# Optimization experiments

Measured on AMD Instinct MI355X. Metric: run time of the kernel, lower is better.

## Reference

```python
import jax, jax.numpy as jnp
import numpy as np

EMBED_DIM = 1024
NUM_HEADS = 16
HEAD_DIM = EMBED_DIM // NUM_HEADS
L, B, S = 2048, 2, 2048


def setup_inputs() -> dict:
    key = jax.random.key(0)
    k1, k2, k3, k4, k5, k6, k7 = jax.random.split(key, 7)
    query = jax.random.normal(k1, (L, B, EMBED_DIM), dtype=jnp.float32)
    kk = jax.random.normal(k2, (S, B, EMBED_DIM), dtype=jnp.float32)
    vv = jax.random.normal(k3, (S, B, EMBED_DIM), dtype=jnp.float32)
    # in_proj: Linear(E, 3E) -> weight (3E, E), bias (3E,)
    w_in = jax.random.normal(k4, (3 * EMBED_DIM, EMBED_DIM), dtype=jnp.float32) * (1.0 / np.sqrt(EMBED_DIM))
    b_in = jax.random.normal(k5, (3 * EMBED_DIM,), dtype=jnp.float32) * 0.02
    w_out = jax.random.normal(k6, (EMBED_DIM, EMBED_DIM), dtype=jnp.float32) * (1.0 / np.sqrt(EMBED_DIM))
    b_out = jax.random.normal(k7, (EMBED_DIM,), dtype=jnp.float32) * 0.02
    return {"query": query, "key": kk, "value": vv,
            "w_in": w_in, "b_in": b_in, "w_out": w_out, "b_out": b_out}


def _split_heads(x, seq_len, batch):
    # (T, B, E) -> (B, H, T, d)
    return x.reshape(seq_len, batch, NUM_HEADS, HEAD_DIM).transpose(1, 2, 0, 3)


def reference(query, key, value, w_in, b_in, w_out, b_out):
    seq_q, batch, _ = query.shape
    seq_kv = key.shape[0]
    # split fused in_proj into q/k/v projections (chunk along output rows)
    wq, wk, wv = jnp.split(w_in, 3, axis=0)
    bq, bk, bv = jnp.split(b_in, 3, axis=0)
    q = query @ wq.T + bq            # (L, B, E)
    k = key @ wk.T + bk              # (S, B, E)
    v = value @ wv.T + bv            # (S, B, E)
    q = _split_heads(q, seq_q, batch)   # (B, H, L, d)
    k = _split_heads(k, seq_kv, batch)  # (B, H, S, d)
    v = _split_heads(v, seq_kv, batch)  # (B, H, S, d)
    scale = jnp.asarray(np.sqrt(HEAD_DIM), dtype=q.dtype)
    scores = jnp.einsum('bhld,bhsd->bhls', q, k) / scale  # (B, H, L, S)
    attn = jax.nn.softmax(scores, axis=-1)
    context = jnp.einsum('bhls,bhsd->bhld', attn, v)      # (B, H, L, d)
    # (B, H, L, d) -> (L, B, E)
    context = context.transpose(2, 0, 1, 3).reshape(seq_q, batch, EMBED_DIM)
    attn_output = context @ w_out.T + b_out
    return attn_output
```

## Files before the change

### kernel.cpp

```cpp
#include <hip/hip_runtime.h>
#include <hip/hip_bf16.h>
#include <stdint.h>

#define L_SEQ 2048
#define S_SEQ 2048
#define BATCH 2
#define EMB 1024
#define NH 16
#define HD 64
#define MROWS 4096

typedef __bf16 bf16x8 __attribute__((ext_vector_type(8)));
typedef float f32x4 __attribute__((ext_vector_type(4)));
typedef __hip_bfloat16 bf16;

__device__ __forceinline__ f32x4 mfma16(bf16x8 a, bf16x8 b, f32x4 c) {
    return __builtin_amdgcn_mfma_f32_16x16x32_bf16(a, b, c, 0, 0, 0);
}

__device__ __forceinline__ void gll16(const bf16* g, bf16* l) {
    __builtin_amdgcn_global_load_lds(
        (const __attribute__((address_space(1))) void*)g,
        (__attribute__((address_space(3))) void*)l, 16, 0, 0);
}

__device__ __forceinline__ bf16x8 ld8_cvt(const float* p) {
    const float4 a = *reinterpret_cast<const float4*>(p);
    const float4 b = *reinterpret_cast<const float4*>(p + 4);
    union { bf16x8 v; bf16 h[8]; } u;
    u.h[0] = __float2bfloat16(a.x); u.h[1] = __float2bfloat16(a.y);
    u.h[2] = __float2bfloat16(a.z); u.h[3] = __float2bfloat16(a.w);
    u.h[4] = __float2bfloat16(b.x); u.h[5] = __float2bfloat16(b.y);
    u.h[6] = __float2bfloat16(b.z); u.h[7] = __float2bfloat16(b.w);
    return u.v;
}

__device__ __forceinline__ uint32_t packbf2(float a, float b) {
    const uint32_t ra = __float_as_uint(a) + 0x8000u;
    const uint32_t rb = __float_as_uint(b) + 0x8000u;
    return __builtin_amdgcn_perm(rb, ra, 0x07060302u);
}

__global__ __launch_bounds__(256) void cvt_kernel(
    const float* __restrict__ w_in, const float* __restrict__ w_out,
    const float* __restrict__ q_in, const float* __restrict__ k_in,
    const float* __restrict__ v_in,
    bf16* __restrict__ wib, bf16* __restrict__ wob,
    bf16* __restrict__ Xq, bf16* __restrict__ Xk, bf16* __restrict__ Xv)
{
    const size_t i = ((size_t)blockIdx.x * 256 + threadIdx.x) * 8;
    const size_t o1 = (size_t)3 * EMB * EMB;
    const size_t o2 = o1 + (size_t)EMB * EMB;
    const size_t o3 = o2 + (size_t)MROWS * EMB;
    const size_t o4 = o3 + (size_t)MROWS * EMB;
    const float* src; bf16* dst; size_t j;
    if      (i < o1) { src = w_in;  dst = wib; j = i; }
    else if (i < o2) { src = w_out; dst = wob; j = i - o1; }
    else if (i < o3) { src = q_in;  dst = Xq;  j = i - o2; }
    else if (i < o4) { src = k_in;  dst = Xk;  j = i - o3; }
    else             { src = v_in;  dst = Xv;  j = i - o4; }
    *reinterpret_cast<bf16x8*>(dst + j) = ld8_cvt(src + j);
}

__global__ __launch_bounds__(256) void qkv_gemm(
    const bf16* __restrict__ Xq, const bf16* __restrict__ Xk,
    const bf16* __restrict__ Xv, const bf16* __restrict__ wib,
    const float* __restrict__ b_in,
    bf16* __restrict__ Qh, bf16* __restrict__ Kh, bf16* __restrict__ Vh)
{
    __shared__ alignas(16) bf16 lds_a[128 * 32];
    __shared__ alignas(16) bf16 lds_b[128 * 32];

    const int tid  = threadIdx.x;
    const int lane = tid & 63;
    const int wv   = tid >> 6;
    const int quad = lane >> 4;
    const int lx   = lane & 15;

    const int m0  = blockIdx.x * 128;
    const int n0g = blockIdx.y * 128;
    const int chunk = n0g >> 10;
    const bf16* Aop = (chunk == 0) ? Xq : (chunk == 1) ? Xk : Xv;

    const int wm = (wv >> 1) * 64;
    const int wn = (wv & 1) * 64;

    const int gr = 16 * wv + (lane >> 2);
    const int gc = (lane & 3) * 8;
    const bf16* gA = Aop + (size_t)(m0 + gr) * EMB + gc;
    const bf16* gB = wib + (size_t)(n0g + gr) * EMB + gc;
    bf16* lA = lds_a + wv * 512;
    bf16* lB = lds_b + wv * 512;

    f32x4 acc[4][4];
#pragma unroll
    for (int i = 0; i < 4; i++)
#pragma unroll
        for (int j = 0; j < 4; j++) acc[i][j] = (f32x4){0.f, 0.f, 0.f, 0.f};

    for (int kt = 0; kt < EMB; kt += 32) {
        __syncthreads();
        gll16(gA + kt, lA);
        gll16(gA + 64 * EMB + kt, lA + 2048);
        gll16(gB + kt, lB);
        gll16(gB + 64 * EMB + kt, lB + 2048);
        __syncthreads();

        bf16x8 af[4], bfv[4];
        const int ka = quad * 8;
#pragma unroll
        for (int sm = 0; sm < 4; sm++)
            af[sm] = *reinterpret_cast<const bf16x8*>(lds_a + (wm + sm * 16 + lx) * 32 + ka);
#pragma unroll
        for (int sn = 0; sn < 4; sn++)
            bfv[sn] = *reinterpret_cast<const bf16x8*>(lds_b + (wn + sn * 16 + lx) * 32 + ka);
#pragma unroll
        for (int sm = 0; sm < 4; sm++)
#pragma unroll
            for (int sn = 0; sn < 4; sn++)
                acc[sm][sn] = mfma16(af[sm], bfv[sn], acc[sm][sn]);
    }

    const float scale = (chunk == 0) ? 0.18033688011112042f : 1.0f;
    bf16* dst = (chunk == 0) ? Qh : (chunk == 1) ? Kh : Vh;
#pragma unroll
    for (int sn = 0; sn < 4; sn++) {
        const int n_g = n0g + wn + sn * 16 + lx;
        const float bias = b_in[n_g];
        const int nc = n_g & (EMB - 1);
        const int h  = nc >> 6;
        const int dd = nc & 63;
#pragma unroll
        for (int sm = 0; sm < 4; sm++) {
#pragma unroll
            for (int r = 0; r < 4; r++) {
                const int m_g = m0 + wm + sm * 16 + quad * 4 + r;
                const int t = m_g >> 1;
                const int b = m_g & 1;
                const int bhidx = b * NH + h;
                const float v = (acc[sm][sn][r] + bias) * scale;
                dst[((size_t)bhidx * S_SEQ + t) * HD + dd] = __float2bfloat16(v);
            }
        }
    }
}

#define TST 72
__global__ __launch_bounds__(256) void transpose_v(
    const bf16* __restrict__ Vh, bf16* __restrict__ Vt)
{
    __shared__ alignas(16) bf16 t[64 * TST];
    const int tid = threadIdx.x;
    const int bh  = blockIdx.y;
    const int s0  = blockIdx.x * 64;
    const int r0  = tid >> 3;
    const int c0  = (tid & 7) * 8;

    const bf16* src = Vh + (size_t)bh * S_SEQ * HD;
    uint4 a = *reinterpret_cast<const uint4*>(src + (size_t)(s0 + r0) * HD + c0);
    uint4 b = *reinterpret_cast<const uint4*>(src + (size_t)(s0 + r0 + 32) * HD + c0);
    *reinterpret_cast<uint4*>(t + r0 * TST + c0) = a;
    *reinterpret_cast<uint4*>(t + (r0 + 32) * TST + c0) = b;
    __syncthreads();

    const int sc = (tid & 7) * 8;
    bf16* dst = Vt + (size_t)bh * HD * S_SEQ;
#pragma unroll
    for (int half = 0; half < 2; half++) {
        const int d = (tid >> 3) + half * 32;
        union { bf16 h[8]; uint4 u; } o;
#pragma unroll
        for (int j = 0; j < 8; j++) o.h[j] = t[(sc + j) * TST + d];
        *reinterpret_cast<uint4*>(dst + (size_t)d * S_SEQ + s0 + sc) = o.u;
    }
}

__global__ __launch_bounds__(512, 4) void attn_kernel(
    const bf16* __restrict__ Qh, const bf16* __restrict__ Kh,
    const bf16* __restrict__ Vt, bf16* __restrict__ ctx)
{
    __shared__ alignas(16) bf16 k_lds[128 * 64];
    __shared__ alignas(16) bf16 v_lds[64 * 128];

    const int tid  = threadIdx.x;
    const int lane = tid & 63;
    const int wv   = tid >> 6;
    const int quad = lane >> 4;
    const int lx   = lane & 15;
    const int lx7  = lane & 7;

    const int bh = blockIdx.y;
    const int l0 = blockIdx.x * 128;
    const int q0 = wv * 16;

    const bf16* Kbase = Kh + (size_t)bh * S_SEQ * HD;
    const bf16* Vbase = Vt + (size_t)bh * HD * S_SEQ;

    const bf16* qrow = Qh + ((size_t)bh * L_SEQ + l0 + q0 + lx) * HD + quad * 8;
    const bf16x8 qf0 = *reinterpret_cast<const bf16x8*>(qrow);
    const bf16x8 qf1 = *reinterpret_cast<const bf16x8*>(qrow + 32);

    float m_run = -1e30f, l_run = 0.f;
    f32x4 accv[4];
#pragma unroll
    for (int sn = 0; sn < 4; sn++) accv[sn] = (f32x4){0.f, 0.f, 0.f, 0.f};

    const int kr0 = tid >> 3;
    const int kc  = (tid & 7) * 8;
    const int vd0 = tid >> 4;
    const int vs  = (tid & 15) * 8;
    const int ksw = (((kc >> 3) ^ (kr0 & 7)) << 3);
    const int vsw = (((vs >> 3) ^ (vd0 & 7)) << 3);

    uint4 ka = *reinterpret_cast<const uint4*>(Kbase + (size_t)kr0 * HD + kc);
    uint4 kb = *reinterpret_cast<const uint4*>(Kbase + (size_t)(kr0 + 64) * HD + kc);
    uint4 va = *reinterpret_cast<const uint4*>(Vbase + (size_t)vd0 * S_SEQ + vs);
    uint4 vb = *reinterpret_cast<const uint4*>(Vbase + (size_t)(vd0 + 32) * S_SEQ + vs);

    for (int s0 = 0; s0 < S_SEQ; s0 += 128) {
        __syncthreads();
        *reinterpret_cast<uint4*>(k_lds + kr0 * 64 + ksw) = ka;
        *reinterpret_cast<uint4*>(k_lds + (kr0 + 64) * 64 + ksw) = kb;
        *reinterpret_cast<uint4*>(v_lds + vd0 * 128 + vsw) = va;
        *reinterpret_cast<uint4*>(v_lds + (vd0 + 32) * 128 + vsw) = vb;
        __syncthreads();

        const int s1 = (s0 + 128) & (S_SEQ - 1);
        ka = *reinterpret_cast<const uint4*>(Kbase + (size_t)(s1 + kr0) * HD + kc);
        kb = *reinterpret_cast<const uint4*>(Kbase + (size_t)(s1 + kr0 + 64) * HD + kc);
        va = *reinterpret_cast<const uint4*>(Vbase + (size_t)vd0 * S_SEQ + s1 + vs);
        vb = *reinterpret_cast<const uint4*>(Vbase + (size_t)(vd0 + 32) * S_SEQ + s1 + vs);

        f32x4 sc[8];
#pragma unroll
        for (int c = 0; c < 8; c++) {
            const bf16* kr = k_lds + (c * 16 + lx) * 64;
            bf16x8 kf0 = *reinterpret_cast<const bf16x8*>(kr + ((quad ^ lx7) << 3));
            bf16x8 kf1 = *reinterpret_cast<const bf16x8*>(kr + (((quad + 4) ^ lx7) << 3));
            f32x4 tt = (f32x4){0.f, 0.f, 0.f, 0.f};
            tt = mfma16(kf0, qf0, tt);
            tt = mfma16(kf1, qf1, tt);
            sc[c] = tt;
        }

        f32x4 vm = sc[0];
#pragma unroll
        for (int c = 1; c < 8; c++)
#pragma unroll
            for (int r = 0; r < 4; r++) vm[r] = fmaxf(vm[r], sc[c][r]);
        float mloc = fmaxf(fmaxf(vm[0], vm[1]), fmaxf(vm[2], vm[3]));
        mloc = fmaxf(mloc, __shfl_xor(mloc, 16));
        mloc = fmaxf(mloc, __shfl_xor(mloc, 32));
        const float mnew = fmaxf(m_run, mloc);
        const float al = __builtin_amdgcn_exp2f(m_run - mnew);
        m_run = mnew;

        const f32x4 mnew4 = (f32x4){mnew, mnew, mnew, mnew};
        f32x4 rv = (f32x4){0.f, 0.f, 0.f, 0.f};
#pragma unroll
        for (int c = 0; c < 8; c++) {
            f32x4 d = sc[c] - mnew4;
#pragma unroll
            for (int r = 0; r < 4; r++) sc[c][r] = __builtin_amdgcn_exp2f(d[r]);
            rv += sc[c];
        }
        float rsum = (rv[0] + rv[1]) + (rv[2] + rv[3]);
        rsum += __shfl_xor(rsum, 16);
        rsum += __shfl_xor(rsum, 32);
        l_run = l_run * al + rsum;

#pragma unroll
        for (int r = 0; r < 4; r++) {
            const float ar = __shfl(al, quad * 20 + r);
#pragma unroll
            for (int sn = 0; sn < 4; sn++) accv[sn][r] *= ar;
        }

        uint32_t pk0[8], pk1[8];
#pragma unroll
        for (int c = 0; c < 8; c++) {
            pk0[c] = packbf2(sc[c][0], sc[c][1]);
            pk1[c] = packbf2(sc[c][2], sc[c][3]);
        }

#pragma unroll
        for (int sk = 0; sk < 4; sk++) {
            auto t0 = __builtin_amdgcn_permlane32_swap(pk0[2 * sk], pk0[2 * sk + 1], false, false);
            auto a02 = __builtin_amdgcn_permlane16_swap(t0[0], t0[1], false, false);
            auto t1 = __builtin_amdgcn_permlane32_swap(pk1[2 * sk], pk1[2 * sk + 1], false, false);
            auto a13 = __builtin_amdgcn_permlane16_swap(t1[0], t1[1], false, false);
            union { uint32_t u[4]; bf16x8 v; } pf;
            pf.u[0] = a02[0]; pf.u[1] = a13[0]; pf.u[2] = a02[1]; pf.u[3] = a13[1];
#pragma unroll
            for (int sn = 0; sn < 4; sn++) {
                const bf16* vr = v_lds + (sn * 16 + lx) * 128 + ((((sk * 4 + quad) ^ lx7)) << 3);
                accv[sn] = mfma16(pf.v, *reinterpret_cast<const bf16x8*>(vr), accv[sn]);
            }
        }
    }

    const int b = bh >> 4;
    const int h = bh & 15;
#pragma unroll
    for (int r = 0; r < 4; r++) {
        const float lr = __shfl(l_run, quad * 20 + r);
        const float inv = 1.f / lr;
        const int l = l0 + q0 + quad * 4 + r;
#pragma unroll
        for (int sn = 0; sn < 4; sn++) {
            const int dd = sn * 16 + lx;
            ctx[(size_t)(l * BATCH + b) * EMB + h * HD + dd] =
                __float2bfloat16(accv[sn][r] * inv);
        }
    }
}

__global__ __launch_bounds__(256) void out_gemm(
    const bf16* __restrict__ ctx, const bf16* __restrict__ wob,
    const float* __restrict__ b_out, float* __restrict__ out)
{
    __shared__ alignas(16) bf16 lds_a[64 * 32];
    __shared__ alignas(16) bf16 lds_b[128 * 32];

    const int tid  = threadIdx.x;
    const int lane = tid & 63;
    const int wv   = tid >> 6;
    const int quad = lane >> 4;
    const int lx   = lane & 15;

    const int m0 = blockIdx.x * 64;
    const int n0 = blockIdx.y * 128;

    const int wm = (wv >> 1) * 32;
    const int wn = (wv & 1) * 64;

    const int gr = 16 * wv + (lane >> 2);
    const int gc = (lane & 3) * 8;
    const bf16* gA = ctx + (size_t)(m0 + gr) * EMB + gc;
    const bf16* gB = wob + (size_t)(n0 + gr) * EMB + gc;
    bf16* lA = lds_a + wv * 512;
    bf16* lB = lds_b + wv * 512;

    f32x4 acc[2][4];
#pragma unroll
    for (int i = 0; i < 2; i++)
#pragma unroll
        for (int j = 0; j < 4; j++) acc[i][j] = (f32x4){0.f, 0.f, 0.f, 0.f};

    for (int kt = 0; kt < EMB; kt += 32) {
        __syncthreads();
        gll16(gA + kt, lA);
        gll16(gB + kt, lB);
        gll16(gB + 64 * EMB + kt, lB + 2048);
        __syncthreads();

        bf16x8 af[2], bfv[4];
        const int ka = quad * 8;
#pragma unroll
        for (int sm = 0; sm < 2; sm++)
            af[sm] = *reinterpret_cast<const bf16x8*>(lds_a + (wm + sm * 16 + lx) * 32 + ka);
#pragma unroll
        for (int sn = 0; sn < 4; sn++)
            bfv[sn] = *reinterpret_cast<const bf16x8*>(lds_b + (wn + sn * 16 + lx) * 32 + ka);
#pragma unroll
        for (int sm = 0; sm < 2; sm++)
#pragma unroll
            for (int sn = 0; sn < 4; sn++)
                acc[sm][sn] = mfma16(af[sm], bfv[sn], acc[sm][sn]);
    }

#pragma unroll
    for (int sn = 0; sn < 4; sn++) {
        const int n_g = n0 + wn + sn * 16 + lx;
        const float bias = b_out[n_g];
#pragma unroll
        for (int sm = 0; sm < 2; sm++) {
#pragma unroll
            for (int r = 0; r < 4; r++) {
                const int m_g = m0 + wm + sm * 16 + quad * 4 + r;
                out[(size_t)m_g * EMB + n_g] = acc[sm][sn][r] + bias;
            }
        }
    }
}

extern "C" void kernel_launch(void* const* d_in, const int* in_sizes, int n_in,
                              void* d_out, int out_size, void* d_ws, size_t ws_size,
                              hipStream_t stream)
{
    const float* query = (const float*)d_in[0];
    const float* key_  = (const float*)d_in[1];
    const float* value = (const float*)d_in[2];
    const float* w_in  = (const float*)d_in[3];
    const float* b_in  = (const float*)d_in[4];
    const float* w_out = (const float*)d_in[5];
    const float* b_out = (const float*)d_in[6];
    float* out = (float*)d_out;

    const size_t seg = (size_t)MROWS * EMB;
    bf16* wib = (bf16*)d_ws;
    bf16* wob = wib + (size_t)3 * EMB * EMB;
    bf16* Xq  = wob + (size_t)EMB * EMB;
    bf16* Xk  = Xq + seg;
    bf16* Xv  = Xk + seg;
    bf16* Qh  = Xv + seg;
    bf16* Kh  = Qh + seg;
    bf16* Vh  = Kh + seg;
    bf16* Vt  = Xq;
    bf16* ctx = Vh;

    cvt_kernel<<<8192, 256, 0, stream>>>(w_in, w_out, query, key_, value,
                                         wib, wob, Xq, Xk, Xv);
    qkv_gemm<<<dim3(32, 24), 256, 0, stream>>>(Xq, Xk, Xv, wib, b_in, Qh, Kh, Vh);
    transpose_v<<<dim3(32, 32), 256, 0, stream>>>(Vh, Vt);
    attn_kernel<<<dim3(16, 32), 512, 0, stream>>>(Qh, Kh, Vt, ctx);
    out_gemm<<<dim3(64, 8), 256, 0, stream>>>(ctx, wob, b_out, out);
}
```

Baseline: 235.4 us.

## Double-buffer K via async global-to-LDS loads and read V directly from global

```diff
diff --git a/kernel.cpp b/kernel.cpp
--- a/kernel.cpp
+++ b/kernel.cpp
@@ -179,8 +179,7 @@
     const bf16* __restrict__ Qh, const bf16* __restrict__ Kh,
     const bf16* __restrict__ Vt, bf16* __restrict__ ctx)
 {
-    __shared__ alignas(16) bf16 k_lds[128 * 64];
-    __shared__ alignas(16) bf16 v_lds[64 * 128];
+    __shared__ alignas(16) bf16 k_lds[2][128 * 64];
 
     const int tid  = threadIdx.x;
     const int lane = tid & 63;
@@ -205,42 +204,49 @@
 #pragma unroll
     for (int sn = 0; sn < 4; sn++) accv[sn] = (f32x4){0.f, 0.f, 0.f, 0.f};
 
-    const int kr0 = tid >> 3;
-    const int kc  = (tid & 7) * 8;
-    const int vd0 = tid >> 4;
-    const int vs  = (tid & 15) * 8;
-    const int ksw = (((kc >> 3) ^ (kr0 & 7)) << 3);
-    const int vsw = (((vs >> 3) ^ (vd0 & 7)) << 3);
-
-    uint4 ka = *reinterpret_cast<const uint4*>(Kbase + (size_t)kr0 * HD + kc);
-    uint4 kb = *reinterpret_cast<const uint4*>(Kbase + (size_t)(kr0 + 64) * HD + kc);
-    uint4 va = *reinterpret_cast<const uint4*>(Vbase + (size_t)vd0 * S_SEQ + vs);
-    uint4 vb = *reinterpret_cast<const uint4*>(Vbase + (size_t)(vd0 + 32) * S_SEQ + vs);
-
+    const int grow  = wv * 16 + (lane >> 3);
+    const int gcol8 = ((lane & 7) ^ (lane >> 3)) << 3;
+    const bf16* gK = Kbase + (size_t)grow * HD + gcol8;
+    bf16* lK0 = &k_lds[0][(wv * 16) * 64];
+    bf16* lK1 = &k_lds[1][(wv * 16) * 64];
+
+    const bf16* vBp[4];
+#pragma unroll
+    for (int sn = 0; sn < 4; sn++)
+        vBp[sn] = Vbase + (size_t)(sn * 16 + lx) * S_SEQ + quad * 8;
+
+    gll16(gK, lK0);
+    gll16(gK + (size_t)8 * HD, lK0 + 8 * 64);
+
+    int cur = 0;
     for (int s0 = 0; s0 < S_SEQ; s0 += 128) {
         __syncthreads();
-        *reinterpret_cast<uint4*>(k_lds + kr0 * 64 + ksw) = ka;
-        *reinterpret_cast<uint4*>(k_lds + (kr0 + 64) * 64 + ksw) = kb;
-        *reinterpret_cast<uint4*>(v_lds + vd0 * 128 + vsw) = va;
-        *reinterpret_cast<uint4*>(v_lds + (vd0 + 32) * 128 + vsw) = vb;
-        __syncthreads();
-
-        const int s1 = (s0 + 128) & (S_SEQ - 1);
-        ka = *reinterpret_cast<const uint4*>(Kbase + (size_t)(s1 + kr0) * HD + kc);
-        kb = *reinterpret_cast<const uint4*>(Kbase + (size_t)(s1 + kr0 + 64) * HD + kc);
-        va = *reinterpret_cast<const uint4*>(Vbase + (size_t)vd0 * S_SEQ + s1 + vs);
-        vb = *reinterpret_cast<const uint4*>(Vbase + (size_t)(vd0 + 32) * S_SEQ + s1 + vs);
+
+        if (s0 + 128 < S_SEQ) {
+            const bf16* gKn = gK + (size_t)(s0 + 128) * HD;
+            bf16* lKn = cur ? lK0 : lK1;
+            gll16(gKn, lKn);
+            gll16(gKn + (size_t)8 * HD, lKn + 8 * 64);
+        }
+        const bf16* kbuf = &k_lds[cur][0];
 
         f32x4 sc[8];
 #pragma unroll
         for (int c = 0; c < 8; c++) {
-            const bf16* kr = k_lds + (c * 16 + lx) * 64;
+            const bf16* kr = kbuf + (c * 16 + lx) * 64;
             bf16x8 kf0 = *reinterpret_cast<const bf16x8*>(kr + ((quad ^ lx7) << 3));
             bf16x8 kf1 = *reinterpret_cast<const bf16x8*>(kr + (((quad + 4) ^ lx7) << 3));
             f32x4 tt = (f32x4){0.f, 0.f, 0.f, 0.f};
             tt = mfma16(kf0, qf0, tt);
             tt = mfma16(kf1, qf1, tt);
             sc[c] = tt;
+        }
+
+        uint4 vg[4][4];
+#pragma unroll
+        for (int sn = 0; sn < 4; sn++) {
+            vg[sn][0] = *reinterpret_cast<const uint4*>(vBp[sn] + s0);
+            vg[sn][1] = *reinterpret_cast<const uint4*>(vBp[sn] + s0 + 32);
         }
 
         f32x4 vm = sc[0];
@@ -284,6 +290,12 @@
         }
 
 #pragma unroll
+        for (int sn = 0; sn < 4; sn++) {
+            vg[sn][2] = *reinterpret_cast<const uint4*>(vBp[sn] + s0 + 64);
+            vg[sn][3] = *reinterpret_cast<const uint4*>(vBp[sn] + s0 + 96);
+        }
+
+#pragma unroll
         for (int sk = 0; sk < 4; sk++) {
             auto t0 = __builtin_amdgcn_permlane32_swap(pk0[2 * sk], pk0[2 * sk + 1], false, false);
             auto a02 = __builtin_amdgcn_permlane16_swap(t0[0], t0[1], false, false);
@@ -293,10 +305,12 @@
             pf.u[0] = a02[0]; pf.u[1] = a13[0]; pf.u[2] = a02[1]; pf.u[3] = a13[1];
 #pragma unroll
             for (int sn = 0; sn < 4; sn++) {
-                const bf16* vr = v_lds + (sn * 16 + lx) * 128 + ((((sk * 4 + quad) ^ lx7)) << 3);
-                accv[sn] = mfma16(pf.v, *reinterpret_cast<const bf16x8*>(vr), accv[sn]);
+                union { uint4 u; bf16x8 v; } vf;
+                vf.u = vg[sn][sk];
+                accv[sn] = mfma16(pf.v, vf.v, accv[sn]);
             }
         }
+        cur ^= 1;
     }
 
     const int b = bh >> 4;
```

Result: slower. 301.8 us (+28.2%).
